# Kernel optimization log

Measured on AMD Instinct MI355X. Metric: run time of the kernel, lower is better.

## Reference

```python
import jax, jax.numpy as jnp
import numpy as np


def _conv_t(z, w, b, pad):
    # z: (1,1,N,T), w: (1,1,1,k), cross-correlation along last axis (as torch Conv2d)
    y = jax.lax.conv_general_dilated(
        z, w, window_strides=(1, 1), padding=pad,
        dimension_numbers=("NCHW", "OIHW", "NCHW"))
    return y + b[None, :, None, None]


def setup_inputs() -> dict:
    key = jax.random.key(0)
    ks = jax.random.split(key, 7)
    N, T, L = 4096, 8192, 4  # L = blocks * layers
    return {
        "x": jax.random.normal(ks[0], (N, T), jnp.float32),
        "start_w": jax.random.normal(ks[1], (1, 1, 1, 1), jnp.float32),
        "start_b": jax.random.normal(ks[2], (1,), jnp.float32),
        "filter_w": jax.random.normal(ks[3], (L, 1, 1, 1, 2), jnp.float32),
        "filter_b": jax.random.normal(ks[4], (L, 1), jnp.float32),
        "gate_w": jax.random.normal(ks[5], (L, 1, 1, 1, 2), jnp.float32),
        "gate_b": jax.random.normal(ks[6], (L, 1), jnp.float32),
    }


def reference(x, start_w, start_b, filter_w, filter_b, gate_w, gate_b):
    # (N,T) -> (1,1,N,T)
    z = x[None, None]
    # start 1x1 conv
    z = _conv_t(z, start_w, start_b, ((0, 0), (0, 0)))
    # torch 'same' padding for kernel=2, dilation=1: (left=0, right=1)
    same_pad = ((0, 0), (0, 1))
    L = filter_w.shape[0]
    for i in range(L):  # small fixed layer count
        f = jnp.tanh(_conv_t(z, filter_w[i], filter_b[i], same_pad))
        g = jax.nn.sigmoid(_conv_t(z, gate_w[i], gate_b[i], same_pad))
        z = f * g
    # squeeze(1) -> permute(0,2,1) -> squeeze -> (T, N)
    out = jnp.transpose(z[0, 0])  # (N,T) -> (T,N)
    return jnp.nan_to_num(out)
```

## Files before the change

kernel.cpp:

```cpp
#include <hip/hip_runtime.h>

typedef float v2f __attribute__((ext_vector_type(2)));

#define NN 4096
#define TTOT 8192

constexpr int S    = 32;
constexpr int HALO = 4;
constexpr int TN   = 64;
constexpr int TB   = 4 * S;

__device__ __forceinline__ float fexp2(float x) {
#if __has_builtin(__builtin_amdgcn_exp2f)
    return __builtin_amdgcn_exp2f(x);
#else
    return exp2f(x);
#endif
}
__device__ __forceinline__ float frcp(float x) {
#if __has_builtin(__builtin_amdgcn_rcpf)
    return __builtin_amdgcn_rcpf(x);
#else
    return 1.0f / x;
#endif
}
__device__ __forceinline__ v2f splat(float x) { v2f r = {x, x}; return r; }

__global__ __launch_bounds__(256, 8) void gdcn_kernel(
    const float* __restrict__ x,
    const float* __restrict__ start_w,
    const float* __restrict__ start_b,
    const float* __restrict__ filter_w,
    const float* __restrict__ filter_b,
    const float* __restrict__ gate_w,
    const float* __restrict__ gate_b,
    float* __restrict__ out)
{
    const int tid = threadIdx.x;
    const int bn  = blockIdx.x & 63;
    const int bt  = blockIdx.x >> 6;
    const int n0  = bn * TN;
    const int t0  = bt * TB;

    const int nl = tid & 63;
    const int ts = tid >> 6;
    const int tbase = t0 + ts * S;

    const float* xr = x + (size_t)(n0 + nl) * TTOT + tbase;

    float v[S + HALO];
    const bool edge = (tbase + S + HALO > TTOT);
    if (!edge) {
        #pragma unroll
        for (int q = 0; q < (S + HALO) / 4; ++q) {
            float4 f4 = *reinterpret_cast<const float4*>(xr + 4 * q);
            v[4*q+0] = f4.x; v[4*q+1] = f4.y; v[4*q+2] = f4.z; v[4*q+3] = f4.w;
        }
    } else {
        #pragma unroll
        for (int s = 0; s < S + HALO; ++s)
            v[s] = (tbase + s < TTOT) ? xr[s] : 0.0f;
    }

    constexpr float LOG2E = 1.4426950408889634f;

    {
        const float sw = start_w[0], sb = start_b[0];
        #pragma unroll
        for (int s = 0; s < S + HALO; ++s) v[s] = fmaf(v[s], sw, sb);
        if (edge) {
            #pragma unroll
            for (int s = 0; s < S + HALO; ++s)
                if (tbase + s >= TTOT) v[s] = 0.0f;
        }
    }

    #pragma unroll
    for (int i = 0; i < 4; ++i) {
        const float ff0 = filter_w[2*i]   * (2.0f * LOG2E);
        const float ff1 = filter_w[2*i+1] * (2.0f * LOG2E);
        const float ffb = filter_b[i]     * (2.0f * LOG2E);
        const float gg0 = -gate_w[2*i]    * LOG2E;
        const float gg1 = -gate_w[2*i+1]  * LOG2E;
        const float ggb = -gate_b[i]      * LOG2E;
        const int len = S + HALO - 1 - i;

        #pragma unroll
        for (int s = 0; s + 1 < len; s += 2) {
            v2f a = { v[s],   v[s+1] };
            v2f b = { v[s+1], v[s+2] };
            v2f tf = a * splat(ff0) + b * splat(ff1) + splat(ffb);
            v2f tg = a * splat(gg0) + b * splat(gg1) + splat(ggb);
            if (i == 0) {
                tf.x = fminf(tf.x, 60.0f); tf.y = fminf(tf.y, 60.0f);
                tg.x = fminf(tg.x, 60.0f); tg.y = fminf(tg.y, 60.0f);
            }
            v2f ef = { fexp2(tf.x), fexp2(tf.y) };
            v2f eg = { fexp2(tg.x), fexp2(tg.y) };
            v2f num = ef - splat(1.0f);
            v2f den = (ef + splat(1.0f)) * (eg + splat(1.0f));
            v2f r   = { frcp(den.x), frcp(den.y) };
            v2f res = num * r;
            v[s] = res.x; v[s+1] = res.y;
        }
        if (len & 1) {
            const int s = len - 1;
            float a = v[s], b = v[s + 1];
            float tf = fmaf(a, ff0, fmaf(b, ff1, ffb));
            float tg = fmaf(a, gg0, fmaf(b, gg1, ggb));
            if (i == 0) { tf = fminf(tf, 60.0f); tg = fminf(tg, 60.0f); }
            float ef = fexp2(tf), eg = fexp2(tg);
            v[s] = (ef - 1.0f) * frcp((ef + 1.0f) * (eg + 1.0f));
        }
        if (edge) {
            #pragma unroll
            for (int s = 0; s < len; ++s)
                if (tbase + s >= TTOT) v[s] = 0.0f;
        }
    }

    float* op = out + (size_t)tbase * NN + n0 + nl;
    #pragma unroll
    for (int s = 0; s < S; ++s)
        op[(size_t)s * NN] = v[s];
}

extern "C" void kernel_launch(void* const* d_in, const int* in_sizes, int n_in,
                              void* d_out, int out_size, void* d_ws, size_t ws_size,
                              hipStream_t stream) {
    const float* x  = (const float*)d_in[0];
    const float* sw = (const float*)d_in[1];
    const float* sb = (const float*)d_in[2];
    const float* fw = (const float*)d_in[3];
    const float* fb = (const float*)d_in[4];
    const float* gw = (const float*)d_in[5];
    const float* gb = (const float*)d_in[6];
    float* out = (float*)d_out;

    dim3 grid((NN / TN) * (TTOT / TB));
    gdcn_kernel<<<grid, 256, 0, stream>>>(x, sw, sb, fw, fb, gw, gb, out);
}
```

Measured before the change: 65.59 us.

## Stage input rows through swizzled LDS for coalesced loads with wider time tiles

Each block now covers 16 rows by 512 time steps. Rows are loaded into LDS with fully coalesced float4 reads (16 threads per row), and each thread then reads its 36-element window from a swizzled LDS layout. Before, each thread read a strided 144-byte chunk directly from global memory. Output stores now write 16 contiguous floats per time step instead of 64, which may hurt store coalescing. The block also uses about 35KB of LDS, and the launch bound drops to 4 blocks per CU.

New measurement: 72.56 us. 10.6% more time.

```diff
diff --git a/kernel.cpp b/kernel.cpp
--- a/kernel.cpp
+++ b/kernel.cpp
@@ -5,10 +5,12 @@
 #define NN 4096
 #define TTOT 8192
 
-constexpr int S    = 32;
-constexpr int HALO = 4;
-constexpr int TN   = 64;
-constexpr int TB   = 4 * S;
+constexpr int S     = 32;
+constexpr int HALO  = 4;
+constexpr int ROWS  = 16;
+constexpr int COLS  = 512;
+constexpr int UNITS = (COLS + HALO + 3) / 4;
+constexpr int PITCHU = 138;
 
 __device__ __forceinline__ float fexp2(float x) {
 #if __has_builtin(__builtin_amdgcn_exp2f)
@@ -26,7 +28,11 @@
 }
 __device__ __forceinline__ v2f splat(float x) { v2f r = {x, x}; return r; }
 
-__global__ __launch_bounds__(256, 8) void gdcn_kernel(
+__device__ __forceinline__ int swz(int r, int u) {
+    return r * PITCHU + (u ^ ((u >> 3) & 7) ^ (r & 7));
+}
+
+__global__ __launch_bounds__(256, 4) void gdcn_kernel(
     const float* __restrict__ x,
     const float* __restrict__ start_w,
     const float* __restrict__ start_b,
@@ -36,30 +42,45 @@
     const float* __restrict__ gate_b,
     float* __restrict__ out)
 {
+    __shared__ float4 lds[ROWS * PITCHU];
+
     const int tid = threadIdx.x;
-    const int bn  = blockIdx.x & 63;
-    const int bt  = blockIdx.x >> 6;
-    const int n0  = bn * TN;
-    const int t0  = bt * TB;
+    const int bn  = blockIdx.x & 255;
+    const int bt  = blockIdx.x >> 8;
+    const int n0  = bn * ROWS;
+    const int t0  = bt * COLS;
+    const bool last = (bt == (TTOT / COLS) - 1);
 
-    const int nl = tid & 63;
-    const int ts = tid >> 6;
-    const int tbase = t0 + ts * S;
+    {
+        const int lr = tid >> 4;
+        const int lu = tid & 15;
+        const float4* xrow =
+            reinterpret_cast<const float4*>(x + (size_t)(n0 + lr) * TTOT + t0);
+        #pragma unroll
+        for (int k = 0; k < 9; ++k) {
+            const int u = lu + 16 * k;
+            if (u < UNITS) {
+                float4 val;
+                if (last && u == UNITS - 1) {
+                    val.x = val.y = val.z = val.w = 0.0f;
+                } else {
+                    val = xrow[u];
+                }
+                lds[swz(lr, u)] = val;
+            }
+        }
+    }
+    __syncthreads();
 
-    const float* xr = x + (size_t)(n0 + nl) * TTOT + tbase;
+    const int cr = tid & 15;
+    const int cj = tid >> 4;
+    const bool edge = last && (cj == 15);
 
     float v[S + HALO];
-    const bool edge = (tbase + S + HALO > TTOT);
-    if (!edge) {
-        #pragma unroll
-        for (int q = 0; q < (S + HALO) / 4; ++q) {
-            float4 f4 = *reinterpret_cast<const float4*>(xr + 4 * q);
-            v[4*q+0] = f4.x; v[4*q+1] = f4.y; v[4*q+2] = f4.z; v[4*q+3] = f4.w;
-        }
-    } else {
-        #pragma unroll
-        for (int s = 0; s < S + HALO; ++s)
-            v[s] = (tbase + s < TTOT) ? xr[s] : 0.0f;
+    #pragma unroll
+    for (int q = 0; q < 9; ++q) {
+        float4 f4 = lds[swz(cr, cj * 8 + q)];
+        v[4*q+0] = f4.x; v[4*q+1] = f4.y; v[4*q+2] = f4.z; v[4*q+3] = f4.w;
     }
 
     constexpr float LOG2E = 1.4426950408889634f;
@@ -70,8 +91,7 @@
         for (int s = 0; s < S + HALO; ++s) v[s] = fmaf(v[s], sw, sb);
         if (edge) {
             #pragma unroll
-            for (int s = 0; s < S + HALO; ++s)
-                if (tbase + s >= TTOT) v[s] = 0.0f;
+            for (int s = S; s < S + HALO; ++s) v[s] = 0.0f;
         }
     }
 
@@ -114,12 +134,11 @@
         }
         if (edge) {
             #pragma unroll
-            for (int s = 0; s < len; ++s)
-                if (tbase + s >= TTOT) v[s] = 0.0f;
+            for (int s = S; s < S + HALO; ++s) v[s] = 0.0f;
         }
     }
 
-    float* op = out + (size_t)tbase * NN + n0 + nl;
+    float* op = out + (size_t)(t0 + cj * S) * NN + n0 + cr;
     #pragma unroll
     for (int s = 0; s < S; ++s)
         op[(size_t)s * NN] = v[s];
@@ -137,6 +156,6 @@
     const float* gb = (const float*)d_in[6];
     float* out = (float*)d_out;
 
-    dim3 grid((NN / TN) * (TTOT / TB));
+    dim3 grid((NN / ROWS) * (TTOT / COLS));
     gdcn_kernel<<<grid, 256, 0, stream>>>(x, sw, sb, fw, fb, gw, gb, out);
 }
```

## Stage input tiles through double-buffered LDS with async global-to-LDS loads

Applied to the files above, without the earlier changes.

The kernel becomes a persistent-style loop. Each block handles 32 rows over a 2048-column chunk in 8 tiles. Input tiles are copied into XOR-swizzled, double-buffered shared memory using global_load_lds, and the next tile's load overlaps the current tile's compute. This replaces per-thread strided float4 loads, whose reads of input rows were uncoalesced, and cuts down on redundant halo loads. The costs are one barrier per tile, lower occupancy from launch bounds of 2 and 64KB of LDS, and fewer blocks (512), which may underfill the device.

Measured after the change: 69.49 us. 5.9% more time.

```diff
diff --git a/kernel.cpp b/kernel.cpp
--- a/kernel.cpp
+++ b/kernel.cpp
@@ -5,10 +5,13 @@
 #define NN 4096
 #define TTOT 8192
 
-constexpr int S    = 32;
-constexpr int HALO = 4;
-constexpr int TN   = 64;
-constexpr int TB   = 4 * S;
+constexpr int ROWS   = 32;
+constexpr int TCOLS  = 256;
+constexpr int UNITS  = 64;
+constexpr int S      = 32;
+constexpr int HALO   = 4;
+constexpr int CTILES = 8;
+constexpr int CHUNK  = TCOLS * CTILES;
 
 __device__ __forceinline__ float fexp2(float x) {
 #if __has_builtin(__builtin_amdgcn_exp2f)
@@ -26,7 +29,13 @@
 }
 __device__ __forceinline__ v2f splat(float x) { v2f r = {x, x}; return r; }
 
-__global__ __launch_bounds__(256, 8) void gdcn_kernel(
+#if __has_builtin(__builtin_amdgcn_global_load_lds)
+#define HAVE_GLD 1
+typedef const __attribute__((address_space(1))) void g_void;
+typedef __attribute__((address_space(3))) void l_void;
+#endif
+
+__global__ __launch_bounds__(256, 2) void gdcn_kernel(
     const float* __restrict__ x,
     const float* __restrict__ start_w,
     const float* __restrict__ start_b,
@@ -36,93 +45,131 @@
     const float* __restrict__ gate_b,
     float* __restrict__ out)
 {
-    const int tid = threadIdx.x;
-    const int bn  = blockIdx.x & 63;
-    const int bt  = blockIdx.x >> 6;
-    const int n0  = bn * TN;
-    const int t0  = bt * TB;
+    __shared__ float4 B[2][ROWS * UNITS];
 
-    const int nl = tid & 63;
-    const int ts = tid >> 6;
-    const int tbase = t0 + ts * S;
+    const int tid  = threadIdx.x;
+    const int nb   = blockIdx.x & 127;
+    const int ch   = blockIdx.x >> 7;
+    const int n0   = nb * ROWS;
+    const int t0   = ch * CHUNK;
 
-    const float* xr = x + (size_t)(n0 + nl) * TTOT + tbase;
+    const int w    = tid >> 6;
+    const int lane = tid & 63;
+    const int cr   = tid & 31;
+    const int cj   = tid >> 5;
+    const int sx   = cr & 7;
 
-    float v[S + HALO];
-    const bool edge = (tbase + S + HALO > TTOT);
-    if (!edge) {
+    constexpr float LOG2E = 1.4426950408889634f;
+    const float sw = start_w[0], sb = start_b[0];
+    float ff0[4], ff1[4], ffb[4], gg0[4], gg1[4], ggb[4];
+    #pragma unroll
+    for (int i = 0; i < 4; ++i) {
+        ff0[i] = filter_w[2*i]   * (2.0f * LOG2E);
+        ff1[i] = filter_w[2*i+1] * (2.0f * LOG2E);
+        ffb[i] = filter_b[i]     * (2.0f * LOG2E);
+        gg0[i] = -gate_w[2*i]    * LOG2E;
+        gg1[i] = -gate_w[2*i+1]  * LOG2E;
+        ggb[i] = -gate_b[i]      * LOG2E;
+    }
+
+    auto stage = [&](int tile, int b) {
+        const float* base = x + (size_t)n0 * TTOT + (t0 + tile * TCOLS);
         #pragma unroll
-        for (int q = 0; q < (S + HALO) / 4; ++q) {
-            float4 f4 = *reinterpret_cast<const float4*>(xr + 4 * q);
+        for (int i = 0; i < 8; ++i) {
+            const int r = i * 4 + w;
+            const float* src = base + (size_t)r * TTOT + ((lane ^ (r & 7)) << 2);
+#ifdef HAVE_GLD
+            __builtin_amdgcn_global_load_lds((g_void*)src,
+                                             (l_void*)&B[b][r * UNITS],
+                                             16, 0, 0);
+#else
+            B[b][r * UNITS + lane] = *reinterpret_cast<const float4*>(src);
+#endif
+        }
+    };
+
+    auto load_halo = [&](int it) -> float4 {
+        float4 h = {0.f, 0.f, 0.f, 0.f};
+        const int th = t0 + (it + 1) * TCOLS;
+        if (cj == 7 && th < TTOT)
+            h = *reinterpret_cast<const float4*>(x + (size_t)(n0 + cr) * TTOT + th);
+        return h;
+    };
+
+    stage(0, 0);
+    float4 hreg = load_halo(0);
+    __syncthreads();
+
+    #pragma unroll 2
+    for (int it = 0; it < CTILES; ++it) {
+        const int cur = it & 1;
+        const int tbase = t0 + it * TCOLS + cj * S;
+        const float4* buf = B[cur];
+        const int rb = cr * UNITS + cj * 8;
+
+        float v[S + HALO];
+        #pragma unroll
+        for (int q = 0; q < 8; ++q) {
+            float4 f4 = buf[rb + (q ^ sx)];
             v[4*q+0] = f4.x; v[4*q+1] = f4.y; v[4*q+2] = f4.z; v[4*q+3] = f4.w;
         }
-    } else {
-        #pragma unroll
-        for (int s = 0; s < S + HALO; ++s)
-            v[s] = (tbase + s < TTOT) ? xr[s] : 0.0f;
-    }
+        {
+            float4 f4;
+            if (cj < 7) f4 = buf[rb + 8 + sx];
+            else        f4 = hreg;
+            v[32] = f4.x; v[33] = f4.y; v[34] = f4.z; v[35] = f4.w;
+        }
 
-    constexpr float LOG2E = 1.4426950408889634f;
+        if (it + 1 < CTILES) {
+            stage(it + 1, cur ^ 1);
+            hreg = load_halo(it + 1);
+        }
 
-    {
-        const float sw = start_w[0], sb = start_b[0];
         #pragma unroll
         for (int s = 0; s < S + HALO; ++s) v[s] = fmaf(v[s], sw, sb);
-        if (edge) {
-            #pragma unroll
-            for (int s = 0; s < S + HALO; ++s)
-                if (tbase + s >= TTOT) v[s] = 0.0f;
-        }
-    }
-
-    #pragma unroll
-    for (int i = 0; i < 4; ++i) {
-        const float ff0 = filter_w[2*i]   * (2.0f * LOG2E);
-        const float ff1 = filter_w[2*i+1] * (2.0f * LOG2E);
-        const float ffb = filter_b[i]     * (2.0f * LOG2E);
-        const float gg0 = -gate_w[2*i]    * LOG2E;
-        const float gg1 = -gate_w[2*i+1]  * LOG2E;
-        const float ggb = -gate_b[i]      * LOG2E;
-        const int len = S + HALO - 1 - i;
+        const bool edge = (tbase + S + HALO > TTOT);
+        if (edge) { v[32] = v[33] = v[34] = v[35] = 0.f; }
 
         #pragma unroll
-        for (int s = 0; s + 1 < len; s += 2) {
-            v2f a = { v[s],   v[s+1] };
-            v2f b = { v[s+1], v[s+2] };
-            v2f tf = a * splat(ff0) + b * splat(ff1) + splat(ffb);
-            v2f tg = a * splat(gg0) + b * splat(gg1) + splat(ggb);
-            if (i == 0) {
-                tf.x = fminf(tf.x, 60.0f); tf.y = fminf(tf.y, 60.0f);
-                tg.x = fminf(tg.x, 60.0f); tg.y = fminf(tg.y, 60.0f);
+        for (int i = 0; i < 4; ++i) {
+            const int len = S + HALO - 1 - i;
+            #pragma unroll
+            for (int s = 0; s + 1 < len; s += 2) {
+                v2f a = { v[s],   v[s+1] };
+                v2f b = { v[s+1], v[s+2] };
+                v2f tf = a * splat(ff0[i]) + b * splat(ff1[i]) + splat(ffb[i]);
+                v2f tg = a * splat(gg0[i]) + b * splat(gg1[i]) + splat(ggb[i]);
+                if (i == 0) {
+                    tf.x = fminf(tf.x, 60.0f); tf.y = fminf(tf.y, 60.0f);
+                    tg.x = fminf(tg.x, 60.0f); tg.y = fminf(tg.y, 60.0f);
+                }
+                v2f ef = { fexp2(tf.x), fexp2(tf.y) };
+                v2f eg = { fexp2(tg.x), fexp2(tg.y) };
+                v2f num = ef - splat(1.0f);
+                v2f den = (ef + splat(1.0f)) * (eg + splat(1.0f));
+                v2f r   = { frcp(den.x), frcp(den.y) };
+                v2f res = num * r;
+                v[s] = res.x; v[s+1] = res.y;
             }
-            v2f ef = { fexp2(tf.x), fexp2(tf.y) };
-            v2f eg = { fexp2(tg.x), fexp2(tg.y) };
-            v2f num = ef - splat(1.0f);
-            v2f den = (ef + splat(1.0f)) * (eg + splat(1.0f));
-            v2f r   = { frcp(den.x), frcp(den.y) };
-            v2f res = num * r;
-            v[s] = res.x; v[s+1] = res.y;
+            if (len & 1) {
+                const int s = len - 1;
+                float a = v[s], b = v[s + 1];
+                float tf = fmaf(a, ff0[i], fmaf(b, ff1[i], ffb[i]));
+                float tg = fmaf(a, gg0[i], fmaf(b, gg1[i], ggb[i]));
+                if (i == 0) { tf = fminf(tf, 60.0f); tg = fminf(tg, 60.0f); }
+                float ef = fexp2(tf), eg = fexp2(tg);
+                v[s] = (ef - 1.0f) * frcp((ef + 1.0f) * (eg + 1.0f));
+            }
+            if (edge) { v[32] = v[33] = v[34] = v[35] = 0.f; }
         }
-        if (len & 1) {
-            const int s = len - 1;
-            float a = v[s], b = v[s + 1];
-            float tf = fmaf(a, ff0, fmaf(b, ff1, ffb));
-            float tg = fmaf(a, gg0, fmaf(b, gg1, ggb));
-            if (i == 0) { tf = fminf(tf, 60.0f); tg = fminf(tg, 60.0f); }
-            float ef = fexp2(tf), eg = fexp2(tg);
-            v[s] = (ef - 1.0f) * frcp((ef + 1.0f) * (eg + 1.0f));
-        }
-        if (edge) {
-            #pragma unroll
-            for (int s = 0; s < len; ++s)
-                if (tbase + s >= TTOT) v[s] = 0.0f;
-        }
+
+        float* op = out + (size_t)tbase * NN + n0 + cr;
+        #pragma unroll
+        for (int s = 0; s < S; ++s)
+            op[(size_t)s * NN] = v[s];
+
+        __syncthreads();
     }
-
-    float* op = out + (size_t)tbase * NN + n0 + nl;
-    #pragma unroll
-    for (int s = 0; s < S; ++s)
-        op[(size_t)s * NN] = v[s];
 }
 
 extern "C" void kernel_launch(void* const* d_in, const int* in_sizes, int n_in,
@@ -137,6 +184,6 @@
     const float* gb = (const float*)d_in[6];
     float* out = (float*)d_out;
 
-    dim3 grid((NN / TN) * (TTOT / TB));
+    dim3 grid((NN / ROWS) * (TTOT / CHUNK));
     gdcn_kernel<<<grid, 256, 0, stream>>>(x, sw, sb, fw, fb, gw, gb, out);
 }
```
